# Performance work log

Measured on AMD Instinct MI355X. Metric: run time of the kernel, lower is better.

The kernel has to match this reference:

```python
import jax, jax.numpy as jnp
import numpy as np

# EctConfig constants
RESOLUTION = 64   # number of threshold steps
RADIUS = 1.1      # thresholds span [-RADIUS, RADIUS]
NUM_BATCHES = 64  # number of point clouds


def setup_inputs() -> dict:
    key = jax.random.key(0)
    k1, k2, k3 = jax.random.split(key, 3)
    N, D, T = 1048576, 3, 64
    x = jax.random.normal(k1, (N, D), dtype=jnp.float32) * 0.5  # points roughly inside radius
    v = jax.random.normal(k2, (D, T), dtype=jnp.float32)
    v = v / jnp.linalg.norm(v, axis=0, keepdims=True)  # unit directions [D, T]
    batch = jnp.sort(jax.random.randint(k3, (N,), 0, NUM_BATCHES)).astype(jnp.int64)
    return {"x": x, "v": v, "batch": batch, "num_batches": NUM_BATCHES}


def reference(x, v, batch, num_batches):
    # Projection of every point onto every direction: [N, T]
    nh = x @ v
    R = RESOLUTION
    T = v.shape[1]
    # Map each projected height to a threshold bin in [0, R-1]
    bins = jnp.clip(
        jnp.floor((nh + RADIUS) / (2.0 * RADIUS) * R), 0, R - 1
    ).astype(jnp.int32)  # [N, T]
    # Fused (batch, bin) index so a single scatter-add builds all histograms
    flat = batch[:, None].astype(jnp.int32) * R + bins  # [N, T]
    counts = jnp.zeros((num_batches * R, T), dtype=jnp.float32)
    counts = counts.at[flat, jnp.arange(T)[None, :]].add(1.0)
    # Cumulative count over thresholds = Euler characteristic curve per direction
    ect = jnp.cumsum(counts.reshape(num_batches, R, T), axis=1)  # [B, R, T]
    return ect
```

## Files before the change

### kernel.cpp

```cpp
#include <hip/hip_runtime.h>

#define RES 64
#define TD 64
#define NB 64
#define BLK 1024
#define WAVES (BLK / 64)
#define CHUNK 2048

__global__ __launch_bounds__(256) void ect_init_kernel(
    const int* __restrict__ batch, int N,
    unsigned* __restrict__ counts, int* __restrict__ offs)
{
    int gid = blockIdx.x * 256 + threadIdx.x;
    counts[gid] = 0u;
    if (blockIdx.x == 0 && threadIdx.x <= NB) {
        int val = (int)threadIdx.x;
        int lo = 0, hi = N;
        while (lo < hi) {
            int mid = (lo + hi) >> 1;
            if (batch[mid] < val) lo = mid + 1; else hi = mid;
        }
        offs[threadIdx.x] = lo;
    }
}

__global__ __launch_bounds__(BLK) void ect_hist_kernel(
    const float* __restrict__ x, const float* __restrict__ v,
    const int* __restrict__ offs, unsigned* __restrict__ counts, int N)
{
    const int start = blockIdx.x * CHUNK;
    const int stop  = min(start + CHUNK, N);
    if (start >= N) return;

    __shared__ unsigned hist[RES * TD];

    const int t = threadIdx.x & 63;
    const int w = threadIdx.x >> 6;
    const float S = 64.0f / 2.2f;
    const float v0S = v[t] * S;
    const float v1S = v[TD + t] * S;
    const float v2S = v[2 * TD + t] * S;

    int lo = 0, hi = NB;
    while (lo < hi) {
        int mid = (lo + hi + 1) >> 1;
        if (offs[mid] <= start) lo = mid; else hi = mid - 1;
    }
    int b = lo;

#define SELREG(q) ((q) < 64 ? l0 : ((q) < 128 ? l1 : l2))
#define RD(q) __uint_as_float(__builtin_amdgcn_readlane(__float_as_uint(SELREG(q)), (q) & 63))
#define PROC(j) {                                                      \
        float x0 = RD(3*(j)), x1 = RD(3*(j)+1), x2 = RD(3*(j)+2);      \
        float f = fmaf(x0, v0S, fmaf(x1, v1S, fmaf(x2, v2S, 32.0f)));  \
        f = __builtin_amdgcn_fmed3f(f, 0.0f, 63.0f);                   \
        int bin = (int)f;                                              \
        atomicAdd(&hist[(bin << 6) + t], 1u); }

    int seg = start;
    while (seg < stop) {
        while (offs[b + 1] <= seg) ++b;
        const int segend = min(stop, offs[b + 1]);

        for (int i = threadIdx.x; i < RES * TD; i += BLK) hist[i] = 0u;
        __syncthreads();

        const int ntiles = (segend - seg + 63) >> 6;
        for (int tile = w; tile < ntiles; tile += WAVES) {
            const int p0 = seg + (tile << 6);
            const int cnt = min(64, segend - p0);
            const int fb = 3 * p0 + t;
            float l0, l1, l2;
            if (cnt == 64) {
                l0 = x[fb]; l1 = x[fb + 64]; l2 = x[fb + 128];
                #pragma unroll
                for (int j = 0; j < 64; ++j) PROC(j);
            } else {
                const int lim = 3 * segend;
                l0 = (fb       < lim) ? x[fb]       : 0.0f;
                l1 = (fb +  64 < lim) ? x[fb +  64] : 0.0f;
                l2 = (fb + 128 < lim) ? x[fb + 128] : 0.0f;
                #pragma unroll
                for (int j = 0; j < 64; ++j) {
                    if (j < cnt) PROC(j);
                }
            }
        }
        __syncthreads();

        unsigned* __restrict__ gb = counts + b * (RES * TD);
        for (int i = threadIdx.x; i < RES * TD; i += BLK) {
            unsigned h = hist[i];
            if (h) atomicAdd(&gb[i], h);
        }
        if (segend < stop) __syncthreads();
        seg = segend;
    }
#undef PROC
#undef RD
#undef SELREG
}

__global__ __launch_bounds__(256) void ect_cumsum_kernel(unsigned* __restrict__ u)
{
    int gid = blockIdx.x * 256 + threadIdx.x;
    int b = gid >> 6, t = gid & 63;
    int base = b * (RES * TD) + t;

    unsigned vals[RES];
    #pragma unroll
    for (int r = 0; r < RES; ++r) vals[r] = u[base + (r << 6)];

    unsigned acc = 0u;
    #pragma unroll
    for (int r = 0; r < RES; ++r) {
        acc += vals[r];
        u[base + (r << 6)] = __float_as_uint((float)acc);
    }
}

extern "C" void kernel_launch(void* const* d_in, const int* in_sizes, int n_in,
                              void* d_out, int out_size, void* d_ws, size_t ws_size,
                              hipStream_t stream) {
    const float* x = (const float*)d_in[0];
    const float* v = (const float*)d_in[1];
    const int* batch = (const int*)d_in[2];
    const int N = in_sizes[2];
    int* offs = (int*)d_ws;

    ect_init_kernel<<<(NB * RES * TD) / 256, 256, 0, stream>>>(
        batch, N, (unsigned*)d_out, offs);

    const int nblocks = (N + CHUNK - 1) / CHUNK;
    ect_hist_kernel<<<nblocks, BLK, 0, stream>>>(x, v, offs, (unsigned*)d_out, N);

    ect_cumsum_kernel<<<(NB * TD) / 256, 256, 0, stream>>>((unsigned*)d_out);
}
```

Measured before the change: 35.90 us.

## Split LDS histogram into two copies, prefetch next tile, separate tail handling

The histogram kernel now keeps two shared-memory histogram copies, each serving half the waves, to reduce LDS atomic contention, and sums them at flush time. Each wave prefetches the next full tile of points into registers while binning the current one, so global load latency overlaps the atomic work. Partial tiles go to a single dedicated tail path. The cumsum kernel is relaunched as 64 blocks of 64 threads. The cost is more LDS usage, a larger zeroing loop and higher register pressure from the prefetch registers.

```diff
diff --git a/kernel.cpp b/kernel.cpp
--- a/kernel.cpp
+++ b/kernel.cpp
@@ -4,7 +4,7 @@
 #define TD 64
 #define NB 64
 #define BLK 1024
-#define WAVES (BLK / 64)
+#define WAVES 16
 #define CHUNK 2048
 
 __global__ __launch_bounds__(256) void ect_init_kernel(
@@ -32,10 +32,11 @@
     const int stop  = min(start + CHUNK, N);
     if (start >= N) return;
 
-    __shared__ unsigned hist[RES * TD];
+    __shared__ unsigned hist[2][RES * TD];
 
     const int t = threadIdx.x & 63;
     const int w = threadIdx.x >> 6;
+    unsigned* __restrict__ hw = hist[w >> 3];
     const float S = 64.0f / 2.2f;
     const float v0S = v[t] * S;
     const float v1S = v[TD + t] * S;
@@ -48,63 +49,75 @@
     }
     int b = lo;
 
-#define SELREG(q) ((q) < 64 ? l0 : ((q) < 128 ? l1 : l2))
-#define RD(q) __uint_as_float(__builtin_amdgcn_readlane(__float_as_uint(SELREG(q)), (q) & 63))
-#define PROC(j) {                                                      \
-        float x0 = RD(3*(j)), x1 = RD(3*(j)+1), x2 = RD(3*(j)+2);      \
-        float f = fmaf(x0, v0S, fmaf(x1, v1S, fmaf(x2, v2S, 32.0f)));  \
-        f = __builtin_amdgcn_fmed3f(f, 0.0f, 63.0f);                   \
-        int bin = (int)f;                                              \
-        atomicAdd(&hist[(bin << 6) + t], 1u); }
+#define SELREG(q, r0, r1, r2) ((q) < 64 ? (r0) : ((q) < 128 ? (r1) : (r2)))
+#define RD(q, r0, r1, r2) __uint_as_float(__builtin_amdgcn_readlane(           \
+        __float_as_uint(SELREG(q, r0, r1, r2)), (q) & 63))
+#define PROC1(j, r0, r1, r2) {                                                 \
+        float x0 = RD(3*(j), r0,r1,r2), x1 = RD(3*(j)+1, r0,r1,r2),            \
+              x2 = RD(3*(j)+2, r0,r1,r2);                                      \
+        float f = fmaf(x0, v0S, fmaf(x1, v1S, fmaf(x2, v2S, 32.0f)));          \
+        f = __builtin_amdgcn_fmed3f(f, 0.0f, 63.0f);                           \
+        int bin = (int)f;                                                      \
+        atomicAdd(&hw[(bin << 6) + t], 1u); }
 
     int seg = start;
     while (seg < stop) {
         while (offs[b + 1] <= seg) ++b;
         const int segend = min(stop, offs[b + 1]);
 
-        for (int i = threadIdx.x; i < RES * TD; i += BLK) hist[i] = 0u;
+        for (int i = threadIdx.x; i < 2 * RES * TD; i += BLK) hist[0][i] = 0u;
         __syncthreads();
 
-        const int ntiles = (segend - seg + 63) >> 6;
-        for (int tile = w; tile < ntiles; tile += WAVES) {
-            const int p0 = seg + (tile << 6);
-            const int cnt = min(64, segend - p0);
-            const int fb = 3 * p0 + t;
-            float l0, l1, l2;
-            if (cnt == 64) {
-                l0 = x[fb]; l1 = x[fb + 64]; l2 = x[fb + 128];
-                #pragma unroll
-                for (int j = 0; j < 64; ++j) PROC(j);
-            } else {
-                const int lim = 3 * segend;
-                l0 = (fb       < lim) ? x[fb]       : 0.0f;
-                l1 = (fb +  64 < lim) ? x[fb +  64] : 0.0f;
-                l2 = (fb + 128 < lim) ? x[fb + 128] : 0.0f;
-                #pragma unroll
-                for (int j = 0; j < 64; ++j) {
-                    if (j < cnt) PROC(j);
-                }
+        const int npts = segend - seg;
+        const int nf = npts >> 6;
+
+        float c0, c1, c2, n0, n1, n2;
+        int tl = w;
+        if (tl < nf) {
+            const int fb = 3 * (seg + (tl << 6)) + t;
+            c0 = x[fb]; c1 = x[fb + 64]; c2 = x[fb + 128];
+        }
+        for (; tl < nf; tl += WAVES) {
+            const int tn = tl + WAVES;
+            if (tn < nf) {
+                const int fb = 3 * (seg + (tn << 6)) + t;
+                n0 = x[fb]; n1 = x[fb + 64]; n2 = x[fb + 128];
+            }
+            #pragma unroll
+            for (int j = 0; j < 64; ++j) PROC1(j, c0, c1, c2);
+            if (tn < nf) { c0 = n0; c1 = n1; c2 = n2; }
+        }
+
+        const int rem = npts & 63;
+        if (rem && w == (nf & (WAVES - 1))) {
+            const int fb = 3 * (seg + (nf << 6)) + t;
+            const int lim = 3 * segend;
+            float l0 = (fb       < lim) ? x[fb]       : 0.0f;
+            float l1 = (fb +  64 < lim) ? x[fb +  64] : 0.0f;
+            float l2 = (fb + 128 < lim) ? x[fb + 128] : 0.0f;
+            #pragma unroll
+            for (int j = 0; j < 64; ++j) {
+                if (j < rem) PROC1(j, l0, l1, l2);
             }
         }
         __syncthreads();
 
         unsigned* __restrict__ gb = counts + b * (RES * TD);
         for (int i = threadIdx.x; i < RES * TD; i += BLK) {
-            unsigned h = hist[i];
+            unsigned h = hist[0][i] + hist[1][i];
             if (h) atomicAdd(&gb[i], h);
         }
         if (segend < stop) __syncthreads();
         seg = segend;
     }
-#undef PROC
+#undef PROC1
 #undef RD
 #undef SELREG
 }
 
-__global__ __launch_bounds__(256) void ect_cumsum_kernel(unsigned* __restrict__ u)
+__global__ __launch_bounds__(64) void ect_cumsum_kernel(unsigned* __restrict__ u)
 {
-    int gid = blockIdx.x * 256 + threadIdx.x;
-    int b = gid >> 6, t = gid & 63;
+    int b = blockIdx.x, t = threadIdx.x;
     int base = b * (RES * TD) + t;
 
     unsigned vals[RES];
@@ -134,5 +147,5 @@
     const int nblocks = (N + CHUNK - 1) / CHUNK;
     ect_hist_kernel<<<nblocks, BLK, 0, stream>>>(x, v, offs, (unsigned*)d_out, N);
 
-    ect_cumsum_kernel<<<(NB * TD) / 256, 256, 0, stream>>>((unsigned*)d_out);
+    ect_cumsum_kernel<<<NB, 64, 0, stream>>>((unsigned*)d_out);
 }
```

New measurement: 33.89 us. 1.06x faster.
